# Optimization experiments

Measured on AMD Instinct MI355X. Metric: run time of the kernel, lower is better.

Reference implementation:

```python
import jax, jax.numpy as jnp
import numpy as np

D_MODEL = 1024
N_HEADS = 16
D_K = D_MODEL // N_HEADS
TEMP = 0.01
THRESH = 0.019
NEG_INF = -1e9


def setup_inputs() -> dict:
    key = jax.random.key(0)
    ks = jax.random.split(key, 10)
    B, S = 4, 1024
    # xavier_uniform gain=1 for square [D,D]: limit = sqrt(6/(D+D))
    lim_w = float(np.sqrt(6.0 / (D_MODEL + D_MODEL)))
    # nn.Linear default bias init: U(-1/sqrt(fan_in), 1/sqrt(fan_in))
    lim_b = float(1.0 / np.sqrt(D_MODEL))
    return {
        "user_ID": jax.random.randint(ks[0], (B,), 0, 100000),
        "Q": jax.random.normal(ks[1], (B, S, D_MODEL), jnp.float32),
        "K": jax.random.normal(ks[2], (B, S, D_MODEL), jnp.float32),
        "V": jax.random.normal(ks[3], (B, S, D_MODEL), jnp.float32),
        "Wq": jax.random.uniform(ks[4], (D_MODEL, D_MODEL), jnp.float32, -lim_w, lim_w),
        "bq": jax.random.uniform(ks[5], (D_MODEL,), jnp.float32, -lim_b, lim_b),
        "Wk": jax.random.uniform(ks[6], (D_MODEL, D_MODEL), jnp.float32, -lim_w, lim_w),
        "bk": jax.random.uniform(ks[7], (D_MODEL,), jnp.float32, -lim_b, lim_b),
        "Wv": jax.random.uniform(ks[8], (D_MODEL, D_MODEL), jnp.float32, -lim_w, lim_w),
        "bv": jax.random.uniform(ks[9], (D_MODEL,), jnp.float32, -lim_b, lim_b),
    }


def _split_heads(x):
    B, S, _ = x.shape
    return x.reshape(B, S, N_HEADS, D_K).transpose(0, 2, 1, 3)  # [B,H,S,Dk]


def reference(user_ID, Q, K, V, Wq, bq, Wk, bk, Wv, bv):
    # nn.Linear: y = x @ W.T + b
    q = _split_heads(Q @ Wq.T + bq)
    k = _split_heads(K @ Wk.T + bk)
    v = _split_heads(V @ Wv.T + bv)
    scores = jnp.einsum("bhqd,bhkd->bhqk", q, k) / jnp.sqrt(jnp.float32(D_K))
    # temperature-sharpened softmax used only to build the sparse mask
    attn_sharp = jax.nn.softmax(scores / TEMP, axis=-1)
    mask_sparse = attn_sharp < THRESH
    scores = jnp.where(mask_sparse, jnp.float32(NEG_INF), scores)
    attn = jax.nn.softmax(scores, axis=-1)
    ctx = jnp.einsum("bhqk,bhkd->bhqd", attn, v)
    B, H, S, Dk = ctx.shape
    return ctx.transpose(0, 2, 1, 3).reshape(B, S, H * Dk)
```

## Files before the change

kernel.cpp:

```cpp
#include <hip/hip_runtime.h>

constexpr int D = 1024;
constexpr int S = 1024;
constexpr int NB = 4;
constexpr int NH = 16;
constexpr int DK = 64;
constexpr float THRESH = 0.019f;
constexpr int ROWS = 8;
constexpr int SSP = 1044;

typedef __attribute__((ext_vector_type(8))) short bf16x8;
typedef __attribute__((ext_vector_type(4))) float f32x4;

__device__ __forceinline__ float wave_max(float v) {
#pragma unroll
    for (int off = 32; off >= 1; off >>= 1)
        v = fmaxf(v, __shfl_xor(v, off, 64));
    return v;
}
__device__ __forceinline__ float wave_sum(float v) {
#pragma unroll
    for (int off = 32; off >= 1; off >>= 1)
        v += __shfl_xor(v, off, 64);
    return v;
}

__device__ __forceinline__ int cvtpk(float lo, float hi) {
    int r;
    asm("v_cvt_pk_bf16_f32 %0, %1, %2" : "=v"(r) : "v"(lo), "v"(hi));
    return r;
}
__device__ __forceinline__ bf16x8 pack_bf8(float4 a, float4 b) {
    union { int i[4]; bf16x8 v; } u;
    u.i[0] = cvtpk(a.x, a.y);
    u.i[1] = cvtpk(a.z, a.w);
    u.i[2] = cvtpk(b.x, b.y);
    u.i[3] = cvtpk(b.z, b.w);
    return u.v;
}

__global__ __launch_bounds__(256) void proj_fused(
    const float* __restrict__ Qi, const float* __restrict__ Ki, const float* __restrict__ Vi,
    const float* __restrict__ Wq, const float* __restrict__ bq,
    const float* __restrict__ Wk, const float* __restrict__ bk,
    const float* __restrict__ Wv, const float* __restrict__ bv,
    float* __restrict__ qo, float* __restrict__ ko, float* __restrict__ vo)
{
    __shared__ __align__(16) union SM {
        struct { float Xs[2][16][132]; float Ws[2][16][132]; } f;
        struct { short Ah[128][40];    short Bh[128][40];    } v;
    } sm;

    const int bid = blockIdx.x;
    const int t   = threadIdx.x;

    if (bid < 512) {
        const int pz = bid >> 8;
        const int rb = bid & 255;
        const int n0 = (rb & 7) * 128;
        const int m0 = (rb >> 3) * 128;

        const float* __restrict__ X    = (pz == 0) ? Qi : Ki;
        const float* __restrict__ W    = (pz == 0) ? Wq : Wk;
        const float* __restrict__ bias = (pz == 0) ? bq : bk;

        const int tx = t & 15;
        const int ty = t >> 4;
        const int lr = t >> 1;
        const int lc = (t & 1) << 3;

        const float* __restrict__ Xp = X + (size_t)(m0 + lr) * D + lc;
        const float* __restrict__ Wp = W + (size_t)(n0 + lr) * D + lc;

        float4 xa = *(const float4*)(Xp + 0);
        float4 xb = *(const float4*)(Xp + 4);
        float4 wa = *(const float4*)(Wp + 0);
        float4 wb = *(const float4*)(Wp + 4);
        sm.f.Xs[0][lc + 0][lr] = xa.x; sm.f.Xs[0][lc + 1][lr] = xa.y; sm.f.Xs[0][lc + 2][lr] = xa.z; sm.f.Xs[0][lc + 3][lr] = xa.w;
        sm.f.Xs[0][lc + 4][lr] = xb.x; sm.f.Xs[0][lc + 5][lr] = xb.y; sm.f.Xs[0][lc + 6][lr] = xb.z; sm.f.Xs[0][lc + 7][lr] = xb.w;
        sm.f.Ws[0][lc + 0][lr] = wa.x; sm.f.Ws[0][lc + 1][lr] = wa.y; sm.f.Ws[0][lc + 2][lr] = wa.z; sm.f.Ws[0][lc + 3][lr] = wa.w;
        sm.f.Ws[0][lc + 4][lr] = wb.x; sm.f.Ws[0][lc + 5][lr] = wb.y; sm.f.Ws[0][lc + 6][lr] = wb.z; sm.f.Ws[0][lc + 7][lr] = wb.w;
        __syncthreads();

        float acc[8][8] = {};
        int buf = 0;

        for (int k0 = 0; k0 < D; k0 += 16) {
            const bool more = (k0 + 16) < D;
            if (more) {
                xa = *(const float4*)(Xp + k0 + 16);
                xb = *(const float4*)(Xp + k0 + 20);
                wa = *(const float4*)(Wp + k0 + 16);
                wb = *(const float4*)(Wp + k0 + 20);
            }
#pragma unroll
            for (int kk = 0; kk < 16; ++kk) {
                float4 a0 = *(const float4*)&sm.f.Xs[buf][kk][(ty << 2)];
                float4 a1 = *(const float4*)&sm.f.Xs[buf][kk][64 + (ty << 2)];
                float4 b0 = *(const float4*)&sm.f.Ws[buf][kk][(tx << 2)];
                float4 b1 = *(const float4*)&sm.f.Ws[buf][kk][64 + (tx << 2)];
                float av[8]  = {a0.x, a0.y, a0.z, a0.w, a1.x, a1.y, a1.z, a1.w};
                float bv8[8] = {b0.x, b0.y, b0.z, b0.w, b1.x, b1.y, b1.z, b1.w};
#pragma unroll
                for (int i = 0; i < 8; ++i)
#pragma unroll
                    for (int j = 0; j < 8; ++j)
                        acc[i][j] += av[i] * bv8[j];
            }
            if (more) {
                const int nb = buf ^ 1;
                sm.f.Xs[nb][lc + 0][lr] = xa.x; sm.f.Xs[nb][lc + 1][lr] = xa.y; sm.f.Xs[nb][lc + 2][lr] = xa.z; sm.f.Xs[nb][lc + 3][lr] = xa.w;
                sm.f.Xs[nb][lc + 4][lr] = xb.x; sm.f.Xs[nb][lc + 5][lr] = xb.y; sm.f.Xs[nb][lc + 6][lr] = xb.z; sm.f.Xs[nb][lc + 7][lr] = xb.w;
                sm.f.Ws[nb][lc + 0][lr] = wa.x; sm.f.Ws[nb][lc + 1][lr] = wa.y; sm.f.Ws[nb][lc + 2][lr] = wa.z; sm.f.Ws[nb][lc + 3][lr] = wa.w;
                sm.f.Ws[nb][lc + 4][lr] = wb.x; sm.f.Ws[nb][lc + 5][lr] = wb.y; sm.f.Ws[nb][lc + 6][lr] = wb.z; sm.f.Ws[nb][lc + 7][lr] = wb.w;
                __syncthreads();
                buf = nb;
            }
        }

        const int bb2 = m0 >> 10;
        if (pz == 1) {
            const int s_base = (m0 & 1023) + (ty << 2);
#pragma unroll
            for (int g = 0; g < 2; ++g) {
                const int hh = (n0 >> 6) + g;
#pragma unroll
                for (int jj = 0; jj < 4; ++jj) {
                    const int d = (tx << 2) + jj;
                    const int j = (g << 2) + jj;
                    const float bj = bias[n0 + (g << 6) + d];
                    float* op = &ko[(((size_t)bb2 * NH + hh) * DK + d) * S];
                    *(float4*)(op + s_base) =
                        make_float4(acc[0][j] + bj, acc[1][j] + bj, acc[2][j] + bj, acc[3][j] + bj);
                    *(float4*)(op + s_base + 64) =
                        make_float4(acc[4][j] + bj, acc[5][j] + bj, acc[6][j] + bj, acc[7][j] + bj);
                }
            }
        } else {
            float bj[8];
#pragma unroll
            for (int j = 0; j < 8; ++j)
                bj[j] = bias[n0 + ((j >> 2) << 6) + (tx << 2) + (j & 3)];
#pragma unroll
            for (int i = 0; i < 8; ++i) {
                const int sr = (m0 & 1023) + ((i >> 2) << 6) + (ty << 2) + (i & 3);
#pragma unroll
                for (int g = 0; g < 2; ++g) {
                    const int hh = (n0 >> 6) + g;
                    float* op = &qo[(((size_t)bb2 * NH + hh) * S + sr) * DK + (tx << 2)];
                    *(float4*)op = make_float4(acc[i][(g << 2) + 0] + bj[(g << 2) + 0],
                                               acc[i][(g << 2) + 1] + bj[(g << 2) + 1],
                                               acc[i][(g << 2) + 2] + bj[(g << 2) + 2],
                                               acc[i][(g << 2) + 3] + bj[(g << 2) + 3]);
                }
            }
        }
    } else {
        const int vix = bid - 512;
        const int n0 = (vix & 7) * 128;
        const int m0 = (vix >> 3) * 128;
        const int lane = t & 63;
        const int w4 = t >> 6;
        const int wm = w4 >> 1;
        const int wn = w4 & 1;
        const int cr = lane & 15;
        const int gq = lane >> 4;
        const int ar = t >> 1;
        const int ha = (t & 1) * 16;

        const float* __restrict__ Ap = Vi + (size_t)(m0 + ar) * D + ha;
        const float* __restrict__ Bp = Wv + (size_t)(n0 + ar) * D + ha;

        float4 a0 = *(const float4*)(Ap + 0), a1 = *(const float4*)(Ap + 4);
        float4 a2 = *(const float4*)(Ap + 8), a3 = *(const float4*)(Ap + 12);
        float4 b0 = *(const float4*)(Bp + 0), b1 = *(const float4*)(Bp + 4);
        float4 b2 = *(const float4*)(Bp + 8), b3 = *(const float4*)(Bp + 12);

        f32x4 acc[4][4];
#pragma unroll
        for (int mi = 0; mi < 4; ++mi)
#pragma unroll
            for (int nj = 0; nj < 4; ++nj)
                acc[mi][nj] = (f32x4){0.f, 0.f, 0.f, 0.f};

        for (int ks = 0; ks < 32; ++ks) {
            *(int4*)&sm.v.Ah[ar][ha + 0] = make_int4(cvtpk(a0.x, a0.y), cvtpk(a0.z, a0.w),
                                                     cvtpk(a1.x, a1.y), cvtpk(a1.z, a1.w));
            *(int4*)&sm.v.Ah[ar][ha + 8] = make_int4(cvtpk(a2.x, a2.y), cvtpk(a2.z, a2.w),
                                                     cvtpk(a3.x, a3.y), cvtpk(a3.z, a3.w));
            *(int4*)&sm.v.Bh[ar][ha + 0] = make_int4(cvtpk(b0.x, b0.y), cvtpk(b0.z, b0.w),
                                                     cvtpk(b1.x, b1.y), cvtpk(b1.z, b1.w));
            *(int4*)&sm.v.Bh[ar][ha + 8] = make_int4(cvtpk(b2.x, b2.y), cvtpk(b2.z, b2.w),
                                                     cvtpk(b3.x, b3.y), cvtpk(b3.z, b3.w));
            __syncthreads();
            if (ks < 31) {
                a0 = *(const float4*)(Ap + (ks + 1) * 32 + 0);
                a1 = *(const float4*)(Ap + (ks + 1) * 32 + 4);
                a2 = *(const float4*)(Ap + (ks + 1) * 32 + 8);
                a3 = *(const float4*)(Ap + (ks + 1) * 32 + 12);
                b0 = *(const float4*)(Bp + (ks + 1) * 32 + 0);
                b1 = *(const float4*)(Bp + (ks + 1) * 32 + 4);
                b2 = *(const float4*)(Bp + (ks + 1) * 32 + 8);
                b3 = *(const float4*)(Bp + (ks + 1) * 32 + 12);
            }
            bf16x8 af[4];
#pragma unroll
            for (int mi = 0; mi < 4; ++mi)
                af[mi] = *(const bf16x8*)&sm.v.Ah[64 * wm + 16 * mi + cr][gq * 8];
#pragma unroll
            for (int nj = 0; nj < 4; ++nj) {
                bf16x8 bf = *(const bf16x8*)&sm.v.Bh[64 * wn + 16 * nj + cr][gq * 8];
#pragma unroll
                for (int mi = 0; mi < 4; ++mi)
                    acc[mi][nj] = __builtin_amdgcn_mfma_f32_16x16x32_bf16(af[mi], bf, acc[mi][nj], 0, 0, 0);
            }
            __syncthreads();
        }

        const int bb = m0 >> 10;
#pragma unroll
        for (int nj = 0; nj < 4; ++nj) {
            const int n = n0 + 64 * wn + 16 * nj + cr;
            const float bj = bv[n];
            const int hh = n >> 6, dk = n & 63;
#pragma unroll
            for (int mi = 0; mi < 4; ++mi) {
                const int s0 = (m0 & 1023) + 64 * wm + 16 * mi + gq * 4;
#pragma unroll
                for (int reg = 0; reg < 4; ++reg)
                    vo[(((size_t)bb * NH + hh) * S + s0 + reg) * DK + dk] = acc[mi][nj][reg] + bj;
            }
        }
    }
}

__global__ __launch_bounds__(256) void attn_kernel(
    const float* __restrict__ qw, const float* __restrict__ kw,
    const float* __restrict__ vw, float* __restrict__ out)
{
    __shared__ __align__(16) float ss[ROWS][SSP];
    __shared__ __align__(16) float qT[DK][ROWS];
    __shared__ float rowinv[ROWS];

    const int t    = threadIdx.x;
    const int lane = t & 63;
    const int w    = t >> 6;

    const int L   = blockIdx.x + (S / ROWS) * (blockIdx.y + NH * blockIdx.z);
    const int swz = (L & 7) * ((S / ROWS) * NH * NB / 8) + (L >> 3);
    const int qx  = swz & (S / ROWS - 1);
    const int h   = (swz >> 7) & (NH - 1);
    const int b   = swz >> 11;

    const size_t base = ((size_t)b * NH + h) * S * DK;
    const float* __restrict__ qp = qw + base;
    const float* __restrict__ kp = kw + base;
    const float* __restrict__ vp = vw + base;
    const int q0 = qx * ROWS;

#pragma unroll
    for (int p = 0; p < 2; ++p) {
        int e = t + 256 * p;
        int d = e >> 3, r = e & 7;
        qT[d][r] = qp[(size_t)(q0 + r) * DK + d] * 0.125f;
    }
    __syncthreads();

    float accf[ROWS][4] = {};
    const float* __restrict__ kTb = kp + 4 * t;

    float4 kbuf[4];
#pragma unroll
    for (int d = 0; d < 4; ++d)
        kbuf[d] = *(const float4*)&kTb[(size_t)d * S];

#pragma unroll
    for (int d0 = 0; d0 < DK; d0 += 4) {
        float4 kc[4] = {kbuf[0], kbuf[1], kbuf[2], kbuf[3]};
        if (d0 < DK - 4) {
#pragma unroll
            for (int d = 0; d < 4; ++d)
                kbuf[d] = *(const float4*)&kTb[(size_t)(d0 + 4 + d) * S];
        }
#pragma unroll
        for (int dd = 0; dd < 4; ++dd) {
            const int d = d0 + dd;
            float4 qa = *(const float4*)&qT[d][0];
            float4 qb = *(const float4*)&qT[d][4];
            float qr[8] = {qa.x, qa.y, qa.z, qa.w, qb.x, qb.y, qb.z, qb.w};
            float k4[4] = {kc[dd].x, kc[dd].y, kc[dd].z, kc[dd].w};
#pragma unroll
            for (int r = 0; r < ROWS; ++r)
#pragma unroll
                for (int i = 0; i < 4; ++i)
                    accf[r][i] += qr[r] * k4[i];
        }
    }
#pragma unroll
    for (int r = 0; r < ROWS; ++r)
        *(float4*)&ss[r][4 * t] = make_float4(accf[r][0], accf[r][1], accf[r][2], accf[r][3]);
    __syncthreads();

    for (int rr = w; rr < ROWS; rr += 4) {
        float mx = -3.4e38f;
#pragma unroll
        for (int p = 0; p < S / 64; ++p)
            mx = fmaxf(mx, ss[rr][lane + 64 * p]);
        mx = wave_max(mx);

        float zs = 0.f;
#pragma unroll
        for (int p = 0; p < S / 64; ++p)
            zs += __expf(100.f * (ss[rr][lane + 64 * p] - mx));
        zs = wave_sum(zs);

        const bool any = !((1.0f / zs) < THRESH);

        float z2 = 0.f;
#pragma unroll
        for (int p = 0; p < S / 64; ++p) {
            float x = ss[rr][lane + 64 * p];
            float e = __expf(100.f * (x - mx));
            bool keep = !((e / zs) < THRESH);
            float e2 = any ? (keep ? __expf(x - mx) : 0.f) : 1.f;
            z2 += e2;
            ss[rr][lane + 64 * p] = e2;
        }
        z2 = wave_sum(z2);
        if (lane == 0) rowinv[rr] = 1.0f / z2;
    }
    __syncthreads();

    {
        const int cr = lane & 15;
        const int gq = lane >> 4;
        const float* __restrict__ vB = vp + (size_t)(gq * 8) * DK + (w * 16 + cr);
        const float* __restrict__ arow = &ss[lane & 7][gq * 8];

        float bnx[8];
#pragma unroll
        for (int jj = 0; jj < 8; ++jj) bnx[jj] = vB[(size_t)jj * DK];

        f32x4 acc4 = {0.f, 0.f, 0.f, 0.f};
#pragma unroll 4
        for (int ks = 0; ks < 32; ++ks) {
            float bcur[8];
#pragma unroll
            for (int jj = 0; jj < 8; ++jj) bcur[jj] = bnx[jj];
            if (ks < 31) {
#pragma unroll
                for (int jj = 0; jj < 8; ++jj)
                    bnx[jj] = vB[(size_t)((ks + 1) * 32 + jj) * DK];
            }
            float4 a0 = *(const float4*)&arow[ks * 32];
            float4 a1 = *(const float4*)&arow[ks * 32 + 4];
            bf16x8 af = pack_bf8(a0, a1);
            bf16x8 bf = pack_bf8(make_float4(bcur[0], bcur[1], bcur[2], bcur[3]),
                                 make_float4(bcur[4], bcur[5], bcur[6], bcur[7]));
            acc4 = __builtin_amdgcn_mfma_f32_16x16x32_bf16(af, bf, acc4, 0, 0, 0);
        }

        if (gq < 2) {
            const int dcol = h * DK + w * 16 + cr;
#pragma unroll
            for (int reg = 0; reg < 4; ++reg) {
                const int r = gq * 4 + reg;
                out[((size_t)b * S + q0 + r) * D + dcol] = acc4[reg] * rowinv[r];
            }
        }
    }
}

extern "C" void kernel_launch(void* const* d_in, const int* in_sizes, int n_in,
                              void* d_out, int out_size, void* d_ws, size_t ws_size,
                              hipStream_t stream) {
    const float* Qi = (const float*)d_in[1];
    const float* Ki = (const float*)d_in[2];
    const float* Vi = (const float*)d_in[3];
    const float* Wq = (const float*)d_in[4];
    const float* bq = (const float*)d_in[5];
    const float* Wk = (const float*)d_in[6];
    const float* bk = (const float*)d_in[7];
    const float* Wv = (const float*)d_in[8];
    const float* bv = (const float*)d_in[9];
    float* outp = (float*)d_out;

    float* qws = (float*)d_ws;
    float* kws = qws + (size_t)NB * NH * S * DK;
    float* vws = kws + (size_t)NB * NH * S * DK;

    proj_fused<<<dim3(768), 256, 0, stream>>>(Qi, Ki, Vi, Wq, bq, Wk, bk, Wv, bv,
                                              qws, kws, vws);

    dim3 g2(S / ROWS, NH, NB);
    attn_kernel<<<g2, 256, 0, stream>>>(qws, kws, vws, outp);
}
```

Measured before the change: 580.6 us.

## Rebalance fused projection grid with interleaved smaller V tiles and cache softmax values

The V-projection MFMA path now uses 128x64 tiles instead of 128x128, doubling its block count, and is interleaved with the Q/K FP32 blocks by even/odd block index so the slow and fast blocks mix across CUs. The grid grows from 768 to 1024 blocks and launch bounds request 4 blocks per CU. Separately, the attention sparse-mask pass keeps scores and sharpened exponentials in registers instead of re-reading shared memory and recomputing exp. The trade-off is more register pressure and reloading the V input tile twice per output.

```diff
diff --git a/kernel.cpp b/kernel.cpp
--- a/kernel.cpp
+++ b/kernel.cpp
@@ -39,7 +39,7 @@
     return u.v;
 }
 
-__global__ __launch_bounds__(256) void proj_fused(
+__global__ __launch_bounds__(256, 4) void proj_fused(
     const float* __restrict__ Qi, const float* __restrict__ Ki, const float* __restrict__ Vi,
     const float* __restrict__ Wq, const float* __restrict__ bq,
     const float* __restrict__ Wk, const float* __restrict__ bk,
@@ -48,17 +48,18 @@
 {
     __shared__ __align__(16) union SM {
         struct { float Xs[2][16][132]; float Ws[2][16][132]; } f;
-        struct { short Ah[128][40];    short Bh[128][40];    } v;
+        struct { short Ah[128][40];    short Bh[64][40];     } v;
     } sm;
 
     const int bid = blockIdx.x;
     const int t   = threadIdx.x;
 
-    if (bid < 512) {
-        const int pz = bid >> 8;
-        const int rb = bid & 255;
-        const int n0 = (rb & 7) * 128;
-        const int m0 = (rb >> 3) * 128;
+    if ((bid & 1) == 0) {
+        const int fix = bid >> 1;
+        const int pz  = fix >> 8;
+        const int rb  = fix & 255;
+        const int n0  = (rb & 7) * 128;
+        const int m0  = (rb >> 3) * 128;
 
         const float* __restrict__ X    = (pz == 0) ? Qi : Ki;
         const float* __restrict__ W    = (pz == 0) ? Wq : Wk;
@@ -156,31 +157,31 @@
             }
         }
     } else {
-        const int vix = bid - 512;
-        const int n0 = (vix & 7) * 128;
-        const int m0 = (vix >> 3) * 128;
+        const int vix = bid >> 1;
+        const int n0  = (vix & 15) * 64;
+        const int m0  = (vix >> 4) * 128;
+
         const int lane = t & 63;
-        const int w4 = t >> 6;
-        const int wm = w4 >> 1;
-        const int wn = w4 & 1;
-        const int cr = lane & 15;
-        const int gq = lane >> 4;
-        const int ar = t >> 1;
-        const int ha = (t & 1) * 16;
-
+        const int w    = t >> 6;
+        const int wm   = w >> 1;
+        const int wn   = w & 1;
+        const int cr   = lane & 15;
+        const int gq   = lane >> 4;
+
+        const int ar = t >> 1, ha = (t & 1) * 16;
+        const int br = t >> 2, bq2 = (t & 3) * 8;
         const float* __restrict__ Ap = Vi + (size_t)(m0 + ar) * D + ha;
-        const float* __restrict__ Bp = Wv + (size_t)(n0 + ar) * D + ha;
-
-        float4 a0 = *(const float4*)(Ap + 0), a1 = *(const float4*)(Ap + 4);
-        float4 a2 = *(const float4*)(Ap + 8), a3 = *(const float4*)(Ap + 12);
-        float4 b0 = *(const float4*)(Bp + 0), b1 = *(const float4*)(Bp + 4);
-        float4 b2 = *(const float4*)(Bp + 8), b3 = *(const float4*)(Bp + 12);
-
-        f32x4 acc[4][4];
+        const float* __restrict__ Bp = Wv + (size_t)(n0 + br) * D + bq2;
+
+        float4 a0 = *(const float4*)(Ap + 0),  a1 = *(const float4*)(Ap + 4);
+        float4 a2 = *(const float4*)(Ap + 8),  a3 = *(const float4*)(Ap + 12);
+        float4 b0 = *(const float4*)(Bp + 0),  b1 = *(const float4*)(Bp + 4);
+
+        f32x4 acc[4][2];
 #pragma unroll
         for (int mi = 0; mi < 4; ++mi)
 #pragma unroll
-            for (int nj = 0; nj < 4; ++nj)
+            for (int nj = 0; nj < 2; ++nj)
                 acc[mi][nj] = (f32x4){0.f, 0.f, 0.f, 0.f};
 
         for (int ks = 0; ks < 32; ++ks) {
@@ -188,10 +189,8 @@
                                                      cvtpk(a1.x, a1.y), cvtpk(a1.z, a1.w));
             *(int4*)&sm.v.Ah[ar][ha + 8] = make_int4(cvtpk(a2.x, a2.y), cvtpk(a2.z, a2.w),
                                                      cvtpk(a3.x, a3.y), cvtpk(a3.z, a3.w));
-            *(int4*)&sm.v.Bh[ar][ha + 0] = make_int4(cvtpk(b0.x, b0.y), cvtpk(b0.z, b0.w),
+            *(int4*)&sm.v.Bh[br][bq2]    = make_int4(cvtpk(b0.x, b0.y), cvtpk(b0.z, b0.w),
                                                      cvtpk(b1.x, b1.y), cvtpk(b1.z, b1.w));
-            *(int4*)&sm.v.Bh[ar][ha + 8] = make_int4(cvtpk(b2.x, b2.y), cvtpk(b2.z, b2.w),
-                                                     cvtpk(b3.x, b3.y), cvtpk(b3.z, b3.w));
             __syncthreads();
             if (ks < 31) {
                 a0 = *(const float4*)(Ap + (ks + 1) * 32 + 0);
@@ -200,16 +199,14 @@
                 a3 = *(const float4*)(Ap + (ks + 1) * 32 + 12);
                 b0 = *(const float4*)(Bp + (ks + 1) * 32 + 0);
                 b1 = *(const float4*)(Bp + (ks + 1) * 32 + 4);
-                b2 = *(const float4*)(Bp + (ks + 1) * 32 + 8);
-                b3 = *(const float4*)(Bp + (ks + 1) * 32 + 12);
             }
             bf16x8 af[4];
 #pragma unroll
             for (int mi = 0; mi < 4; ++mi)
                 af[mi] = *(const bf16x8*)&sm.v.Ah[64 * wm + 16 * mi + cr][gq * 8];
 #pragma unroll
-            for (int nj = 0; nj < 4; ++nj) {
-                bf16x8 bf = *(const bf16x8*)&sm.v.Bh[64 * wn + 16 * nj + cr][gq * 8];
+            for (int nj = 0; nj < 2; ++nj) {
+                bf16x8 bf = *(const bf16x8*)&sm.v.Bh[32 * wn + 16 * nj + cr][gq * 8];
 #pragma unroll
                 for (int mi = 0; mi < 4; ++mi)
                     acc[mi][nj] = __builtin_amdgcn_mfma_f32_16x16x32_bf16(af[mi], bf, acc[mi][nj], 0, 0, 0);
@@ -218,11 +215,11 @@
         }
 
         const int bb = m0 >> 10;
-#pragma unroll
-        for (int nj = 0; nj < 4; ++nj) {
-            const int n = n0 + 64 * wn + 16 * nj + cr;
-            const float bj = bv[n];
-            const int hh = n >> 6, dk = n & 63;
+        const int hh = n0 >> 6;
+#pragma unroll
+        for (int nj = 0; nj < 2; ++nj) {
+            const int dk = 32 * wn + 16 * nj + cr;
+            const float bj = bv[n0 + dk];
 #pragma unroll
             for (int mi = 0; mi < 4; ++mi) {
                 const int s0 = (m0 & 1023) + 64 * wm + 16 * mi + gq * 4;
@@ -302,16 +299,21 @@
     __syncthreads();
 
     for (int rr = w; rr < ROWS; rr += 4) {
+        float xv[16], ev[16];
         float mx = -3.4e38f;
 #pragma unroll
-        for (int p = 0; p < S / 64; ++p)
-            mx = fmaxf(mx, ss[rr][lane + 64 * p]);
+        for (int p = 0; p < S / 64; ++p) {
+            xv[p] = ss[rr][lane + 64 * p];
+            mx = fmaxf(mx, xv[p]);
+        }
         mx = wave_max(mx);
 
         float zs = 0.f;
 #pragma unroll
-        for (int p = 0; p < S / 64; ++p)
-            zs += __expf(100.f * (ss[rr][lane + 64 * p] - mx));
+        for (int p = 0; p < S / 64; ++p) {
+            ev[p] = __expf(100.f * (xv[p] - mx));
+            zs += ev[p];
+        }
         zs = wave_sum(zs);
 
         const bool any = !((1.0f / zs) < THRESH);
@@ -319,10 +321,8 @@
         float z2 = 0.f;
 #pragma unroll
         for (int p = 0; p < S / 64; ++p) {
-            float x = ss[rr][lane + 64 * p];
-            float e = __expf(100.f * (x - mx));
-            bool keep = !((e / zs) < THRESH);
-            float e2 = any ? (keep ? __expf(x - mx) : 0.f) : 1.f;
+            bool keep = !((ev[p] / zs) < THRESH);
+            float e2 = any ? (keep ? __expf(xv[p] - mx) : 0.f) : 1.f;
             z2 += e2;
             ss[rr][lane + 64 * p] = e2;
         }
@@ -389,8 +389,8 @@
     float* kws = qws + (size_t)NB * NH * S * DK;
     float* vws = kws + (size_t)NB * NH * S * DK;
 
-    proj_fused<<<dim3(768), 256, 0, stream>>>(Qi, Ki, Vi, Wq, bq, Wk, bk, Wv, bv,
-                                              qws, kws, vws);
+    proj_fused<<<dim3(1024), 256, 0, stream>>>(Qi, Ki, Vi, Wq, bq, Wk, bk, Wv, bv,
+                                               qws, kws, vws);
 
     dim3 g2(S / ROWS, NH, NB);
     attn_kernel<<<g2, 256, 0, stream>>>(qws, kws, vws, outp);
```

After: 2.097 ms. +261.2%, slower.
